# Kernel optimization log

Measured on AMD Instinct MI355X. Metric: run time of the kernel, lower is better.

Reference implementation:

```python
import jax, jax.numpy as jnp
import numpy as np

N_TOKENS = 8192      # codebook size K
HIDDEN = 256         # hidden_size H
N = 8192             # batch of latent vectors (vmapped dim)
COMMITMENT_COST = 0.25


def setup_inputs() -> dict:
    key = jax.random.key(0)
    k_h, k_cb, _ = jax.random.split(key, 3)
    h = jax.random.normal(k_h, (N, HIDDEN), dtype=jnp.float32)
    # codebook initialized exactly as in __init__: normal * 0.1
    codebook = jax.random.normal(k_cb, (N_TOKENS, HIDDEN), dtype=jnp.float32) * 0.1
    temperature = jnp.ones((), dtype=jnp.float32)  # unused, API compat
    return {"h": h, "temperature": temperature, "codebook": codebook}


def reference(h, temperature, codebook):
    """Batched VQ quantization: one-hot nearest-codebook weights + commitment loss.

    h: (N, H) float32, codebook: (K, H) float32. Returns (hard (N,K), loss (N,)).
    """
    del temperature  # VQ is always hard; kept for API compatibility
    K = codebook.shape[0]
    # squared distances ||h - c||^2 = ||h||^2 - 2 h.c + ||c||^2, avoids (N,K,H) tensor
    h_sq = jnp.sum(h * h, axis=-1, keepdims=True)              # (N, 1)
    c_sq = jnp.sum(codebook * codebook, axis=-1)               # (K,)
    dists = h_sq - 2.0 * jnp.einsum('nh,kh->nk', h, codebook) + c_sq[None, :]  # (N, K)
    idx = jnp.argmin(dists, axis=-1)                           # (N,)
    hard = jax.nn.one_hot(idx, K, dtype=h.dtype)               # (N, K)
    # STE wrapping from __call__ (gradient of hard is zero anyway)
    hard = jax.lax.stop_gradient(hard)
    # commitment_loss (per token), matching the module's method
    z_q = codebook[idx]                                        # (N, H) gather
    codebook_loss = jnp.mean((jax.lax.stop_gradient(h) - z_q) ** 2, axis=-1)
    commit_loss = jnp.mean((h - jax.lax.stop_gradient(z_q)) ** 2, axis=-1)
    loss = codebook_loss + COMMITMENT_COST * commit_loss       # (N,)
    return hard, loss
```

## Files before the change

kernel.cpp:

```cpp
#include <hip/hip_runtime.h>
#include <hip/hip_bf16.h>
#include <math.h>

#define N_ROWS   8192
#define K_CODES  8192
#define H_DIM    256
#define NSPLIT   16
#define KSPLIT   (K_CODES / NSPLIT)
#define MARGIN   5e-4f

typedef short short8 __attribute__((ext_vector_type(8)));
typedef float f32x4  __attribute__((ext_vector_type(4)));

#define C2_OFF      0
#define H2_OFF      8192
#define DISTF_OFF   16384
#define IDXF_OFF    (DISTF_OFF + 8192)
#define FCNT_OFF    (IDXF_OFF + 8192)
#define FLIST_OFF   (FCNT_OFF + 16)
#define MAXSLOT     64
#define WS_ZERO_BYTES ((size_t)(FLIST_OFF + MAXSLOT) * 4)

#define PK_AHI ((size_t)0)
#define PK_ALO ((size_t)4 << 20)
#define PK_BHI ((size_t)8 << 20)
#define PK_BLO ((size_t)12 << 20)
#define PART_BEST ((size_t)16 << 20)
#define PART_SEC  (PART_BEST + (size_t)(NSPLIT * N_ROWS * 4))
#define PART_IDX  (PART_SEC  + (size_t)(NSPLIT * N_ROWS * 4))
#define FIXP_BEST (PART_IDX  + (size_t)(NSPLIT * N_ROWS * 4))
#define FIXP_IDX  (FIXP_BEST + (size_t)(MAXSLOT * 64 * 8))
#define SCRATCH_BYTES ((size_t)0x1190000)

__device__ __forceinline__ void async_copy16(const void* g, void* l) {
    __builtin_amdgcn_global_load_lds(
        (const __attribute__((address_space(1))) unsigned int*)g,
        (__attribute__((address_space(3))) unsigned int*)l, 16, 0, 0);
}

__device__ __forceinline__ void conv2(float a, float b, unsigned& hi, unsigned& lo) {
    float2 p0 = make_float2(a, b);
    __hip_bfloat162 hb = __float22bfloat162_rn(p0);
    unsigned h = *(unsigned*)&hb;
    hi = h;
    float ra = a - __uint_as_float(h << 16);
    float rb = b - __uint_as_float(h & 0xFFFF0000u);
    float2 p1 = make_float2(ra, rb);
    __hip_bfloat162 lb = __float22bfloat162_rn(p1);
    lo = *(unsigned*)&lb;
}

__global__ __launch_bounds__(256) void pack_kernel(const float* __restrict__ h,
                                                   const float* __restrict__ cb,
                                                   char* __restrict__ out,
                                                   float* __restrict__ ws) {
    int w    = threadIdx.x >> 6;
    int lane = threadIdx.x & 63;
    int ln15 = lane & 15;
    int kg   = lane >> 4;
    bool isB = blockIdx.x >= 1024;
    int u = ((blockIdx.x & 1023) << 2) + w;
    int p = u >> 3, c = u & 7;
    const float* src = isB ? cb : h;
    char* hiB = out + (isB ? PK_BHI : PK_AHI);
    char* loB = out + (isB ? PK_BLO : PK_ALO);
    const float* s = src + (size_t)(p * 16 + ln15) * H_DIM + c * 32 + kg * 8;
    float4 v0 = *(const float4*)s;
    float4 v1 = *(const float4*)(s + 4);
    unsigned h0, h1, h2, h3, l0, l1, l2, l3;
    conv2(v0.x, v0.y, h0, l0);
    conv2(v0.z, v0.w, h1, l1);
    conv2(v1.x, v1.y, h2, l2);
    conv2(v1.z, v1.w, h3, l3);
    size_t off = ((size_t)u * 64 + lane) * 16;
    *(uint4*)(hiB + off) = make_uint4(h0, h1, h2, h3);
    *(uint4*)(loB + off) = make_uint4(l0, l1, l2, l3);

    float sq = v0.x*v0.x + v0.y*v0.y + v0.z*v0.z + v0.w*v0.w
             + v1.x*v1.x + v1.y*v1.y + v1.z*v1.z + v1.w*v1.w;
    sq += __shfl_xor(sq, 16, 64);
    sq += __shfl_xor(sq, 32, 64);
    if (kg == 0) {
        int row = p * 16 + ln15;
        atomicAdd(&ws[(isB ? C2_OFF : H2_OFF) + row], sq);
    }
}

__global__ __launch_bounds__(256, 3) void vq_min_kernel(const char* __restrict__ pk,
                                                        const float* __restrict__ c2g,
                                                        float* __restrict__ pbest,
                                                        float* __restrict__ psec,
                                                        int* __restrict__ pidx) {
    __shared__ __align__(16) char smem[35840];
    const int tid  = threadIdx.x;
    const int w    = tid >> 6;
    const int lane = tid & 63;
    const int ln15 = lane & 15;
    const int kg   = lane >> 4;
    const int wm   = (w >> 1) * 64;
    const int wn   = (w & 1) * 64;
    const int am   = (w >> 1) * 4;
    const int bn4  = (w & 1) * 4;

    const int rowpan0 = blockIdx.x * 8;
    const int bpan0   = blockIdx.y * (KSPLIT / 16);

    const size_t pkoff = (w == 0) ? PK_AHI : (w == 1) ? PK_ALO : (w == 2) ? PK_BHI : PK_BLO;
    char* lwave = smem + w * 8192;

    float best16[16], sec16[16];
    int   idx16[16];
    #pragma unroll
    for (int t = 0; t < 16; t++) { best16[t] = 3.4e38f; sec16[t] = 3.4e38f; idx16[t] = 0; }

    #pragma unroll 1
    for (int ct = 0; ct < KSPLIT / 128; ++ct) {
        const int kb   = blockIdx.y * KSPLIT + ct * 128;
        const int pan0 = (w < 2) ? rowpan0 : (bpan0 + ct * 8);
        f32x4 acc[4][4];
        #pragma unroll
        for (int i = 0; i < 4; i++)
            #pragma unroll
            for (int j = 0; j < 4; j++) acc[i][j] = (f32x4){0.f, 0.f, 0.f, 0.f};

        #pragma unroll 1
        for (int kc = 0; kc < 8; ++kc) {
            __syncthreads();
            #pragma unroll
            for (int q = 0; q < 8; ++q) {
                const char* g = pk + pkoff + (((size_t)(pan0 + q) * 8 + kc) * 64 + lane) * 16;
                async_copy16(g, lwave + q * 1024);
            }
            __syncthreads();

            short8 bh[4], bl[4];
            #pragma unroll
            for (int j = 0; j < 4; j++) {
                int o = ((bn4 + j) * 64 + lane) * 16;
                bh[j] = *(const short8*)(smem + 16384 + o);
                bl[j] = *(const short8*)(smem + 24576 + o);
            }
            #pragma unroll
            for (int i = 0; i < 4; i++) {
                int o = ((am + i) * 64 + lane) * 16;
                short8 ah = *(const short8*)(smem + o);
                short8 al = *(const short8*)(smem + 8192 + o);
                #pragma unroll
                for (int j = 0; j < 4; j++) {
                    acc[i][j] = __builtin_amdgcn_mfma_f32_16x16x32_bf16(ah, bh[j], acc[i][j], 0, 0, 0);
                    acc[i][j] = __builtin_amdgcn_mfma_f32_16x16x32_bf16(al, bh[j], acc[i][j], 0, 0, 0);
                    acc[i][j] = __builtin_amdgcn_mfma_f32_16x16x32_bf16(ah, bl[j], acc[i][j], 0, 0, 0);
                }
            }
        }

        float cv[4];
        #pragma unroll
        for (int j = 0; j < 4; j++) cv[j] = c2g[kb + wn + j * 16 + ln15];
        #pragma unroll
        for (int i = 0; i < 4; i++)
            #pragma unroll
            for (int reg = 0; reg < 4; reg++) {
                const int t = i * 4 + reg;
                #pragma unroll
                for (int j = 0; j < 4; j++) {
                    float d = cv[j] - 2.f * acc[i][j][reg];
                    int   k = kb + wn + j * 16 + ln15;
                    if (d < best16[t])      { sec16[t] = best16[t]; best16[t] = d; idx16[t] = k; }
                    else if (d < sec16[t])  { sec16[t] = d; }
                }
            }
    }

    #pragma unroll
    for (int t = 0; t < 16; t++) {
        float b = best16[t], s2 = sec16[t];
        int   bi = idx16[t];
        #pragma unroll
        for (int m = 1; m <= 8; m <<= 1) {
            float ob = __shfl_xor(b, m, 64);
            float os = __shfl_xor(s2, m, 64);
            int   oi = __shfl_xor(bi, m, 64);
            if (ob < b)      { s2 = fminf(b, os); b = ob; bi = oi; }
            else if (ob > b) { s2 = fminf(s2, ob); }
            else             { if (oi < bi) bi = oi; s2 = b; }
        }
        best16[t] = b; sec16[t] = s2; idx16[t] = bi;
    }
    float* mb = (float*)(smem + 32768);
    float* ms = (float*)(smem + 32768 + 1024);
    int*   mi = (int*)(smem + 32768 + 2048);
    if (ln15 == 0) {
        #pragma unroll
        for (int i = 0; i < 4; i++)
            #pragma unroll
            for (int reg = 0; reg < 4; reg++) {
                int r = wm + i * 16 + kg * 4 + reg;
                int half = (w & 1);
                mb[r * 2 + half] = best16[i * 4 + reg];
                ms[r * 2 + half] = sec16[i * 4 + reg];
                mi[r * 2 + half] = idx16[i * 4 + reg];
            }
    }
    __syncthreads();
    if (tid < 128) {
        float b  = mb[tid * 2],     s2 = ms[tid * 2];
        int   bi = mi[tid * 2];
        float ob = mb[tid * 2 + 1], os = ms[tid * 2 + 1];
        int   oi = mi[tid * 2 + 1];
        if (ob < b)      { s2 = fminf(b, os); b = ob; bi = oi; }
        else if (ob > b) { s2 = fminf(s2, ob); }
        else             { if (oi < bi) bi = oi; s2 = b; }
        int row = blockIdx.x * 128 + tid;
        int s   = blockIdx.y;
        pbest[s * N_ROWS + row] = b;
        psec [s * N_ROWS + row] = s2;
        pidx [s * N_ROWS + row] = bi;
    }
}

__global__ __launch_bounds__(256) void merge_kernel(const float* __restrict__ pbest,
                                                    const float* __restrict__ psec,
                                                    const int* __restrict__ pidx,
                                                    float* __restrict__ ws) {
    int row = blockIdx.x * blockDim.x + threadIdx.x;
    if (row >= N_ROWS) return;
    float b  = pbest[row];
    float s2 = psec[row];
    int   bi = pidx[row];
    for (int s = 1; s < NSPLIT; s++) {
        float ob = pbest[s * N_ROWS + row];
        float os = psec [s * N_ROWS + row];
        int   oi = pidx [s * N_ROWS + row];
        if (ob < b)      { s2 = fminf(b, os); b = ob; bi = oi; }
        else if (ob > b) { s2 = fminf(s2, ob); }
        else             { if (oi < bi) bi = oi; s2 = b; }
    }
    float h2 = ws[H2_OFF + row];
    ws[DISTF_OFF + row] = h2 + b;
    ((int*)ws)[IDXF_OFF + row] = bi;
    if (s2 - b <= MARGIN) {
        int slot = atomicAdd(&((int*)ws)[FCNT_OFF], 1);
        if (slot < MAXSLOT) ((int*)ws)[FLIST_OFF + slot] = row;
    }
}

__global__ __launch_bounds__(256) void fixup_part(const float* __restrict__ h,
                                                  const float* __restrict__ cb,
                                                  float* __restrict__ ws,
                                                  double* __restrict__ fbest,
                                                  int* __restrict__ fidx) {
    int slot = blockIdx.y;
    int n = ((const int*)ws)[FCNT_OFF];
    if (n > MAXSLOT) n = MAXSLOT;
    if (slot >= n) return;
    int row   = ((const int*)ws)[FLIST_OFF + slot];
    int base  = blockIdx.x * 128;
    int wv    = threadIdx.x >> 6;
    int lane  = threadIdx.x & 63;
    float4 hv = *(const float4*)(h + (size_t)row * H_DIM + lane * 4);

    double best = 1e300;
    int    bi   = 1 << 30;
    for (int c = base + wv; c < base + 128; c += 4) {
        float4 cv = *(const float4*)(cb + (size_t)c * H_DIM + lane * 4);
        float dx = hv.x - cv.x, dy = hv.y - cv.y, dz = hv.z - cv.z, dw = hv.w - cv.w;
        double s = (double)dx * dx + (double)dy * dy + (double)dz * dz + (double)dw * dw;
        #pragma unroll
        for (int off = 32; off > 0; off >>= 1) s += __shfl_down(s, off, 64);
        if (lane == 0 && s < best) { best = s; bi = c; }
    }
    __shared__ double sb[4];
    __shared__ int    si[4];
    if (lane == 0) { sb[wv] = best; si[wv] = bi; }
    __syncthreads();
    if (threadIdx.x == 0) {
        double b = sb[0]; int x = si[0];
        for (int t = 1; t < 4; t++)
            if (sb[t] < b || (sb[t] == b && si[t] < x)) { b = sb[t]; x = si[t]; }
        fbest[slot * 64 + blockIdx.x] = b;
        fidx [slot * 64 + blockIdx.x] = x;
    }
}

__global__ __launch_bounds__(64) void fixup_final(float* __restrict__ ws,
                                                  const double* __restrict__ fbest,
                                                  const int* __restrict__ fidx) {
    int slot = blockIdx.x;
    int n = ((const int*)ws)[FCNT_OFF];
    if (n > MAXSLOT) n = MAXSLOT;
    if (slot >= n) return;
    int lane = threadIdx.x;
    double b = fbest[slot * 64 + lane];
    int    x = fidx [slot * 64 + lane];
    #pragma unroll
    for (int off = 32; off > 0; off >>= 1) {
        double ob = __shfl_down(b, off, 64);
        int    oi = __shfl_down(x, off, 64);
        if (ob < b || (ob == b && oi < x)) { b = ob; x = oi; }
    }
    if (lane == 0) {
        int row = ((const int*)ws)[FLIST_OFF + slot];
        ws[DISTF_OFF + row] = (float)b;
        ((int*)ws)[IDXF_OFF + row] = x;
    }
}

__global__ __launch_bounds__(256) void scatter_kernel(const float* __restrict__ ws,
                                                      float* __restrict__ out) {
    int row = blockIdx.x * 256 + threadIdx.x;
    int bi  = ((const int*)ws)[IDXF_OFF + row];
    out[(size_t)row * K_CODES + bi] = 1.0f;
    out[(size_t)N_ROWS * K_CODES + row] = (1.25f / 256.f) * ws[DISTF_OFF + row];
}

extern "C" void kernel_launch(void* const* d_in, const int* in_sizes, int n_in,
                              void* d_out, int out_size, void* d_ws, size_t ws_size,
                              hipStream_t stream) {
    const float* h  = (const float*)d_in[0];
    const float* cb = (const float*)d_in[2];
    float* out = (float*)d_out;
    float* ws  = (float*)d_ws;
    char*  pk  = (char*)d_out;

    float*  pbest = (float*)(pk + PART_BEST);
    float*  psec  = (float*)(pk + PART_SEC);
    int*    pidx  = (int*)(pk + PART_IDX);
    double* fbest = (double*)(pk + FIXP_BEST);
    int*    fidx  = (int*)(pk + FIXP_IDX);

    hipMemsetAsync(d_ws, 0, WS_ZERO_BYTES, stream);
    pack_kernel<<<2048, 256, 0, stream>>>(h, cb, pk, ws);
    vq_min_kernel<<<dim3(N_ROWS / 128, NSPLIT), 256, 0, stream>>>(pk, ws, pbest, psec, pidx);
    merge_kernel<<<N_ROWS / 256, 256, 0, stream>>>(pbest, psec, pidx, ws);
    fixup_part<<<dim3(64, MAXSLOT), 256, 0, stream>>>(h, cb, ws, fbest, fidx);
    fixup_final<<<MAXSLOT, 64, 0, stream>>>(ws, fbest, fidx);
    hipMemsetAsync(d_out, 0, SCRATCH_BYTES, stream);
    scatter_kernel<<<N_ROWS / 256, 256, 0, stream>>>(ws, out);
}
```

Baseline: 399.0 us.

## Rework VQ distance GEMM into 256x256 tiles with a four-stage async LDS pipeline

Measured after the change: 440.5 us. +10.4%, slower.

```diff
diff --git a/kernel.cpp b/kernel.cpp
--- a/kernel.cpp
+++ b/kernel.cpp
@@ -5,8 +5,7 @@
 #define N_ROWS   8192
 #define K_CODES  8192
 #define H_DIM    256
-#define NSPLIT   16
-#define KSPLIT   (K_CODES / NSPLIT)
+#define NSPLIT2  32
 #define MARGIN   5e-4f
 
 typedef short short8 __attribute__((ext_vector_type(8)));
@@ -26,11 +25,11 @@
 #define PK_BHI ((size_t)8 << 20)
 #define PK_BLO ((size_t)12 << 20)
 #define PART_BEST ((size_t)16 << 20)
-#define PART_SEC  (PART_BEST + (size_t)(NSPLIT * N_ROWS * 4))
-#define PART_IDX  (PART_SEC  + (size_t)(NSPLIT * N_ROWS * 4))
-#define FIXP_BEST (PART_IDX  + (size_t)(NSPLIT * N_ROWS * 4))
+#define PART_SEC  (PART_BEST + (size_t)(NSPLIT2 * N_ROWS * 4))
+#define PART_IDX  (PART_SEC  + (size_t)(NSPLIT2 * N_ROWS * 4))
+#define FIXP_BEST (PART_IDX  + (size_t)(NSPLIT2 * N_ROWS * 4))
 #define FIXP_IDX  (FIXP_BEST + (size_t)(MAXSLOT * 64 * 8))
-#define SCRATCH_BYTES ((size_t)0x1190000)
+#define SCRATCH_BYTES ((size_t)0x1310000)
 
 __device__ __forceinline__ void async_copy16(const void* g, void* l) {
     __builtin_amdgcn_global_load_lds(
@@ -86,136 +85,152 @@
     }
 }
 
-__global__ __launch_bounds__(256, 3) void vq_min_kernel(const char* __restrict__ pk,
+__global__ __launch_bounds__(512, 2) void vq_min_kernel(const char* __restrict__ pk,
                                                         const float* __restrict__ c2g,
                                                         float* __restrict__ pbest,
                                                         float* __restrict__ psec,
                                                         int* __restrict__ pidx) {
-    __shared__ __align__(16) char smem[35840];
+    __shared__ __align__(16) char smem[131072];
     const int tid  = threadIdx.x;
     const int w    = tid >> 6;
     const int lane = tid & 63;
     const int ln15 = lane & 15;
     const int kg   = lane >> 4;
-    const int wm   = (w >> 1) * 64;
-    const int wn   = (w & 1) * 64;
-    const int am   = (w >> 1) * 4;
-    const int bn4  = (w & 1) * 4;
-
-    const int rowpan0 = blockIdx.x * 8;
-    const int bpan0   = blockIdx.y * (KSPLIT / 16);
-
-    const size_t pkoff = (w == 0) ? PK_AHI : (w == 1) ? PK_ALO : (w == 2) ? PK_BHI : PK_BLO;
-    char* lwave = smem + w * 8192;
-
-    float best16[16], sec16[16];
-    int   idx16[16];
+    const int wr   = w >> 2;
+    const int wc   = w & 3;
+    const int wr8  = wr * 8;
+    const int wc4  = wc * 4;
+
+    const int pA0 = blockIdx.x * 16;
+    const int pB0 = blockIdx.y * 16;
+
+    f32x4 acc[8][4];
     #pragma unroll
-    for (int t = 0; t < 16; t++) { best16[t] = 3.4e38f; sec16[t] = 3.4e38f; idx16[t] = 0; }
+    for (int m = 0; m < 8; ++m)
+        #pragma unroll
+        for (int n = 0; n < 4; ++n) acc[m][n] = (f32x4){0.f, 0.f, 0.f, 0.f};
+
+#define STAGE(sE, bufc) do {                                                   \
+    const int ss_ = (sE);                                                      \
+    const int tt_ = ss_ >> 3, cc_ = ss_ & 7;                                   \
+    const char* Ab_ = pk + ((tt_ == 1) ? PK_ALO : PK_AHI);                     \
+    const char* Bb_ = pk + ((tt_ == 2) ? PK_BLO : PK_BHI);                     \
+    char* db_ = smem + (bufc) * 32768;                                         \
+    async_copy16(Ab_ + (((size_t)(pA0 + 2*w)     * 8 + cc_) * 64 + lane) * 16, \
+                 db_ + (2*w)     * 1024);                                      \
+    async_copy16(Ab_ + (((size_t)(pA0 + 2*w + 1) * 8 + cc_) * 64 + lane) * 16, \
+                 db_ + (2*w + 1) * 1024);                                      \
+    async_copy16(Bb_ + (((size_t)(pB0 + 2*w)     * 8 + cc_) * 64 + lane) * 16, \
+                 db_ + 16384 + (2*w)     * 1024);                              \
+    async_copy16(Bb_ + (((size_t)(pB0 + 2*w + 1) * 8 + cc_) * 64 + lane) * 16, \
+                 db_ + 16384 + (2*w + 1) * 1024);                              \
+} while (0)
+
+#define COMPUTE(bufc) do {                                                     \
+    const char* sb_ = smem + (bufc) * 32768;                                   \
+    short8 av[8], bv[4];                                                       \
+    _Pragma("unroll")                                                          \
+    for (int m = 0; m < 8; ++m)                                                \
+        av[m] = *(const short8*)(sb_ + (wr8 + m) * 1024 + lane * 16);          \
+    _Pragma("unroll")                                                          \
+    for (int n = 0; n < 4; ++n)                                                \
+        bv[n] = *(const short8*)(sb_ + 16384 + (wc4 + n) * 1024 + lane * 16);  \
+    __builtin_amdgcn_s_setprio(1);                                             \
+    _Pragma("unroll")                                                          \
+    for (int m = 0; m < 8; ++m)                                                \
+        _Pragma("unroll")                                                      \
+        for (int n = 0; n < 4; ++n)                                            \
+            acc[m][n] = __builtin_amdgcn_mfma_f32_16x16x32_bf16(               \
+                av[m], bv[n], acc[m][n], 0, 0, 0);                             \
+    __builtin_amdgcn_s_setprio(0);                                             \
+} while (0)
+
+#define ITER(sE, bufc, vm) do {                                                \
+    if ((sE) + 2 < 24) STAGE((sE) + 2, ((bufc) + 2) & 3);                      \
+    asm volatile("s_waitcnt vmcnt(" #vm ")" ::: "memory");                     \
+    __builtin_amdgcn_sched_barrier(0);                                         \
+    __builtin_amdgcn_s_barrier();                                              \
+    __builtin_amdgcn_sched_barrier(0);                                         \
+    COMPUTE(bufc);                                                             \
+    __builtin_amdgcn_sched_barrier(0);                                         \
+} while (0)
+
+    STAGE(0, 0);
+    STAGE(1, 1);
 
     #pragma unroll 1
-    for (int ct = 0; ct < KSPLIT / 128; ++ct) {
-        const int kb   = blockIdx.y * KSPLIT + ct * 128;
-        const int pan0 = (w < 2) ? rowpan0 : (bpan0 + ct * 8);
-        f32x4 acc[4][4];
+    for (int sb = 0; sb < 20; sb += 4) {
+        ITER(sb + 0, 0, 8);
+        ITER(sb + 1, 1, 8);
+        ITER(sb + 2, 2, 8);
+        ITER(sb + 3, 3, 8);
+    }
+    ITER(20, 0, 8);
+    ITER(21, 1, 8);
+    ITER(22, 2, 4);
+    ITER(23, 3, 0);
+
+#undef ITER
+#undef COMPUTE
+#undef STAGE
+
+    const int colbase = blockIdx.y * 256 + wc * 64;
+    float cv[4];
+    #pragma unroll
+    for (int n = 0; n < 4; ++n) cv[n] = c2g[colbase + n * 16 + ln15];
+
+    float* mbv = (float*)smem;
+    float* msv = (float*)(smem + 4096);
+    int*   miv = (int*)(smem + 8192);
+
+    #pragma unroll
+    for (int m = 0; m < 8; ++m) {
         #pragma unroll
-        for (int i = 0; i < 4; i++)
+        for (int reg = 0; reg < 4; ++reg) {
+            float b = 3.4e38f, s2 = 3.4e38f;
+            int   bi = 0;
             #pragma unroll
-            for (int j = 0; j < 4; j++) acc[i][j] = (f32x4){0.f, 0.f, 0.f, 0.f};
-
-        #pragma unroll 1
-        for (int kc = 0; kc < 8; ++kc) {
-            __syncthreads();
-            #pragma unroll
-            for (int q = 0; q < 8; ++q) {
-                const char* g = pk + pkoff + (((size_t)(pan0 + q) * 8 + kc) * 64 + lane) * 16;
-                async_copy16(g, lwave + q * 1024);
-            }
-            __syncthreads();
-
-            short8 bh[4], bl[4];
-            #pragma unroll
-            for (int j = 0; j < 4; j++) {
-                int o = ((bn4 + j) * 64 + lane) * 16;
-                bh[j] = *(const short8*)(smem + 16384 + o);
-                bl[j] = *(const short8*)(smem + 24576 + o);
+            for (int n = 0; n < 4; ++n) {
+                float d = cv[n] - 2.f * acc[m][n][reg];
+                int   k = colbase + n * 16 + ln15;
+                if (d < b)       { s2 = b; b = d; bi = k; }
+                else if (d < s2) { s2 = d; }
             }
             #pragma unroll
-            for (int i = 0; i < 4; i++) {
-                int o = ((am + i) * 64 + lane) * 16;
-                short8 ah = *(const short8*)(smem + o);
-                short8 al = *(const short8*)(smem + 8192 + o);
-                #pragma unroll
-                for (int j = 0; j < 4; j++) {
-                    acc[i][j] = __builtin_amdgcn_mfma_f32_16x16x32_bf16(ah, bh[j], acc[i][j], 0, 0, 0);
-                    acc[i][j] = __builtin_amdgcn_mfma_f32_16x16x32_bf16(al, bh[j], acc[i][j], 0, 0, 0);
-                    acc[i][j] = __builtin_amdgcn_mfma_f32_16x16x32_bf16(ah, bl[j], acc[i][j], 0, 0, 0);
-                }
+            for (int msk = 1; msk <= 8; msk <<= 1) {
+                float ob = __shfl_xor(b, msk, 64);
+                float os = __shfl_xor(s2, msk, 64);
+                int   oi = __shfl_xor(bi, msk, 64);
+                if (ob < b)      { s2 = fminf(b, os); b = ob; bi = oi; }
+                else if (ob > b) { s2 = fminf(s2, ob); }
+                else             { if (oi < bi) bi = oi; s2 = b; }
+            }
+            if (ln15 == 0) {
+                int r = wr * 128 + m * 16 + kg * 4 + reg;
+                mbv[r * 4 + wc] = b;
+                msv[r * 4 + wc] = s2;
+                miv[r * 4 + wc] = bi;
             }
         }
-
-        float cv[4];
+    }
+    __syncthreads();
+    if (tid < 256) {
+        float b  = mbv[tid * 4];
+        float s2 = msv[tid * 4];
+        int   bi = miv[tid * 4];
         #pragma unroll
-        for (int j = 0; j < 4; j++) cv[j] = c2g[kb + wn + j * 16 + ln15];
-        #pragma unroll
-        for (int i = 0; i < 4; i++)
-            #pragma unroll
-            for (int reg = 0; reg < 4; reg++) {
-                const int t = i * 4 + reg;
-                #pragma unroll
-                for (int j = 0; j < 4; j++) {
-                    float d = cv[j] - 2.f * acc[i][j][reg];
-                    int   k = kb + wn + j * 16 + ln15;
-                    if (d < best16[t])      { sec16[t] = best16[t]; best16[t] = d; idx16[t] = k; }
-                    else if (d < sec16[t])  { sec16[t] = d; }
-                }
-            }
-    }
-
-    #pragma unroll
-    for (int t = 0; t < 16; t++) {
-        float b = best16[t], s2 = sec16[t];
-        int   bi = idx16[t];
-        #pragma unroll
-        for (int m = 1; m <= 8; m <<= 1) {
-            float ob = __shfl_xor(b, m, 64);
-            float os = __shfl_xor(s2, m, 64);
-            int   oi = __shfl_xor(bi, m, 64);
+        for (int q = 1; q < 4; ++q) {
+            float ob = mbv[tid * 4 + q];
+            float os = msv[tid * 4 + q];
+            int   oi = miv[tid * 4 + q];
             if (ob < b)      { s2 = fminf(b, os); b = ob; bi = oi; }
             else if (ob > b) { s2 = fminf(s2, ob); }
             else             { if (oi < bi) bi = oi; s2 = b; }
         }
-        best16[t] = b; sec16[t] = s2; idx16[t] = bi;
-    }
-    float* mb = (float*)(smem + 32768);
-    float* ms = (float*)(smem + 32768 + 1024);
-    int*   mi = (int*)(smem + 32768 + 2048);
-    if (ln15 == 0) {
-        #pragma unroll
-        for (int i = 0; i < 4; i++)
-            #pragma unroll
-            for (int reg = 0; reg < 4; reg++) {
-                int r = wm + i * 16 + kg * 4 + reg;
-                int half = (w & 1);
-                mb[r * 2 + half] = best16[i * 4 + reg];
-                ms[r * 2 + half] = sec16[i * 4 + reg];
-                mi[r * 2 + half] = idx16[i * 4 + reg];
-            }
-    }
-    __syncthreads();
-    if (tid < 128) {
-        float b  = mb[tid * 2],     s2 = ms[tid * 2];
-        int   bi = mi[tid * 2];
-        float ob = mb[tid * 2 + 1], os = ms[tid * 2 + 1];
-        int   oi = mi[tid * 2 + 1];
-        if (ob < b)      { s2 = fminf(b, os); b = ob; bi = oi; }
-        else if (ob > b) { s2 = fminf(s2, ob); }
-        else             { if (oi < bi) bi = oi; s2 = b; }
-        int row = blockIdx.x * 128 + tid;
-        int s   = blockIdx.y;
-        pbest[s * N_ROWS + row] = b;
-        psec [s * N_ROWS + row] = s2;
-        pidx [s * N_ROWS + row] = bi;
+        int grow = blockIdx.x * 256 + tid;
+        pbest[(size_t)blockIdx.y * N_ROWS + grow] = b;
+        psec [(size_t)blockIdx.y * N_ROWS + grow] = s2;
+        pidx [(size_t)blockIdx.y * N_ROWS + grow] = bi;
     }
 }
 
@@ -228,7 +243,7 @@
     float b  = pbest[row];
     float s2 = psec[row];
     int   bi = pidx[row];
-    for (int s = 1; s < NSPLIT; s++) {
+    for (int s = 1; s < NSPLIT2; s++) {
         float ob = pbest[s * N_ROWS + row];
         float os = psec [s * N_ROWS + row];
         int   oi = pidx [s * N_ROWS + row];
@@ -331,7 +346,7 @@
 
     hipMemsetAsync(d_ws, 0, WS_ZERO_BYTES, stream);
     pack_kernel<<<2048, 256, 0, stream>>>(h, cb, pk, ws);
-    vq_min_kernel<<<dim3(N_ROWS / 128, NSPLIT), 256, 0, stream>>>(pk, ws, pbest, psec, pidx);
+    vq_min_kernel<<<dim3(N_ROWS / 256, NSPLIT2), 512, 0, stream>>>(pk, ws, pbest, psec, pidx);
     merge_kernel<<<N_ROWS / 256, 256, 0, stream>>>(pbest, psec, pidx, ws);
     fixup_part<<<dim3(64, MAXSLOT), 256, 0, stream>>>(h, cb, ws, fbest, fidx);
     fixup_final<<<MAXSLOT, 64, 0, stream>>>(ws, fbest, fidx);
```
